# Kernel tuning notes

Hardware: AMD Instinct MI355X
Metric: run time of the kernel (lower is better)

The kernel has to match this reference:

```python
import jax, jax.numpy as jnp
import numpy as np

LEAKY_ALPHA = 0.2  # LeakyReLU negative slope from init arg `alpha`


def setup_inputs() -> dict:
    key = jax.random.key(0)
    k1, k2, k3, k4 = jax.random.split(key, 4)
    B, N, Fin, Fout = 8, 2048, 256, 256
    h = jax.random.normal(k1, (B, N, Fin), dtype=jnp.float32)
    adj = jax.random.randint(k2, (N, N), 0, 2, dtype=jnp.int32)
    W = jax.random.normal(k3, (Fin, Fout), dtype=jnp.float32) * (1.414 * (6.0 / (Fin + Fout)) ** 0.5)
    a = jax.random.normal(k4, (2 * Fout, 1), dtype=jnp.float32) * (1.414 * (6.0 / (2 * Fout + 1)) ** 0.5)
    return {"h": h, "adj": adj, "W": W, "a": a}


def reference(h, adj, W, a):
    # h: (B, N, Fin), adj: (N, N) int {0,1}, W: (Fin, Fout), a: (2*Fout, 1)
    Fout = W.shape[1]
    Wh = jnp.einsum('bnf,fo->bno', h, W)            # (B, N, Fout)
    a1 = a[:Fout, 0]                                  # attends to target node i
    a2 = a[Fout:, 0]                                  # attends to source node j
    # a^T [Wh_i || Wh_j] == (Wh_i . a1) + (Wh_j . a2); LeakyReLU applied after, as in original
    s_i = Wh @ a1                                     # (B, N)
    s_j = Wh @ a2                                     # (B, N)
    e = jax.nn.leaky_relu(s_i[:, :, None] + s_j[:, None, :], negative_slope=LEAKY_ALPHA)  # (B, N, N)
    N = Wh.shape[1]
    mask = (adj > 0) | jnp.eye(N, dtype=bool)         # adjacency + self-loops
    e = jnp.where(mask[None, :, :], e, -jnp.inf)
    attention = jax.nn.softmax(e, axis=-1)            # dropout is identity in eval
    attention = jnp.nan_to_num(attention, nan=0.0)
    h_prime = jnp.einsum('bij,bjo->bio', attention, Wh)  # (B, N, Fout)
    return jax.nn.elu(h_prime)                        # concat=True -> ELU
```

## Files before the change

kernel.cpp:

```cpp
#include <hip/hip_runtime.h>

typedef unsigned short u16;
typedef unsigned int   u32;
typedef unsigned long long u64;

typedef __bf16 bf16x8 __attribute__((ext_vector_type(8)));
typedef float  f32x4  __attribute__((ext_vector_type(4)));

#define MFMA_BF16(a,b,c) __builtin_amdgcn_mfma_f32_16x16x32_bf16((a),(b),(c),0,0,0)

__device__ __forceinline__ float bf2f(u16 u) {
    return __uint_as_float(((u32)u) << 16);
}
__device__ __forceinline__ u16 f2bf(float x) {
    u32 u = __float_as_uint(x);
    u += 0x7fffu + ((u >> 16) & 1u);
    return (u16)(u >> 16);
}
__device__ __forceinline__ float ldany(const void* p, size_t i, int f32) {
    return f32 ? ((const float*)p)[i] : bf2f(((const u16*)p)[i]);
}
__device__ __forceinline__ int detect_f32(const u32* hw) {
    u32 w = hw[threadIdx.x & 63];
    int e = (w >> 23) & 0xFF;
    u64 m = __ballot(e >= 64 && e <= 190);
    return __popcll(m) >= 32 ? 1 : 0;
}

__global__ __launch_bounds__(256) void kprep(const void* __restrict__ w, const void* __restrict__ a,
                                             const int* __restrict__ adj,
                                             u16* __restrict__ wt, float* __restrict__ wa1,
                                             float* __restrict__ wa2, u64* __restrict__ mb64,
                                             int* __restrict__ cnt, const u32* __restrict__ hw) {
    __shared__ float s1[4], s2[4];
    int bid = blockIdx.x, t = threadIdx.x;
    int wid = t >> 6, lane = t & 63;
    if (bid < 256) {
        if (bid == 0 && t < 8) cnt[t] = 0;
        int f32 = detect_f32(hw);
        int k = bid, o = t;
        float wv = ldany(w, (size_t)k * 256 + o, f32);
        wt[o * 256 + k] = f2bf(wv);
        float p1 = wv * ldany(a, o, f32);
        float p2 = wv * ldany(a, 256 + o, f32);
        for (int d = 32; d; d >>= 1) { p1 += __shfl_down(p1, d); p2 += __shfl_down(p2, d); }
        if (lane == 0) { s1[wid] = p1; s2[wid] = p2; }
        __syncthreads();
        if (o == 0) { wa1[k] = s1[0] + s1[1] + s1[2] + s1[3]; wa2[k] = s2[0] + s2[1] + s2[2] + s2[3]; }
    } else {
        int b2 = bid - 256;
        #pragma unroll
        for (int q = 0; q < 4; q++) {
            int idx = b2 * 16 + wid * 4 + q;
            int mrow = idx >> 5, c = idx & 31;
            int j = c * 64 + lane;
            bool bit = (adj[(size_t)mrow * 2048 + j] > 0) || (j == mrow);
            u64 m = __ballot(bit);
            if (lane == 0) mb64[(size_t)mrow * 32 + c] = m;
        }
    }
}

struct __align__(16) K2LDS {
    u16 At[64 * 68];
    union { u16 Bt[256 * 68]; u16 Ct[256 * 68]; };
    float wa1s[256], wa2s[256];
    float s1[64], s2[64];
};
__global__ __launch_bounds__(512) void k2(const void* __restrict__ h, const u16* __restrict__ wt,
                                          const float* __restrict__ wa1, const float* __restrict__ wa2,
                                          u16* __restrict__ whbt,
                                          float* __restrict__ sig, float* __restrict__ sjg) {
    __shared__ K2LDS L;
    int f32 = detect_f32((const u32*)h);
    int m0 = blockIdx.x * 64;
    int b  = m0 >> 11;
    int n0 = m0 & 2047;
    int t = threadIdx.x;
    int wid = t >> 6, lane = t & 63, ln = lane & 15, qd = lane >> 4;

    if (t < 256) { L.wa1s[t] = wa1[t]; L.wa2s[t] = wa2[t]; }
    if (t < 64) { L.s1[t] = 0.f; L.s2[t] = 0.f; }
    __syncthreads();

    float a1 = 0.f, a2 = 0.f;

    f32x4 acc[4][2];
    for (int mi = 0; mi < 4; mi++)
        for (int ni = 0; ni < 2; ni++)
            acc[mi][ni] = (f32x4){0.f, 0.f, 0.f, 0.f};

    for (int c = 0; c < 4; c++) {
        int k0c = c * 64;
        {
            int r = t >> 3, s = t & 7;
            float xv[8]; u16 uv[8];
            if (f32) {
                const float* src = (const float*)h + (size_t)(m0 + r) * 256 + k0c + s * 8;
                f32x4 x0 = *(const f32x4*)src;
                f32x4 x1 = *(const f32x4*)(src + 4);
                #pragma unroll
                for (int q = 0; q < 4; q++) { xv[q] = x0[q]; xv[4 + q] = x1[q]; }
                #pragma unroll
                for (int q = 0; q < 8; q++) uv[q] = f2bf(xv[q]);
            } else {
                const u16* src = (const u16*)h + (size_t)(m0 + r) * 256 + k0c + s * 8;
                *(uint4*)uv = *(const uint4*)src;
                #pragma unroll
                for (int q = 0; q < 8; q++) xv[q] = bf2f(uv[q]);
            }
            *(uint4*)&L.At[r * 68 + s * 8] = *(uint4*)uv;
            float pa = 0.f, pb = 0.f;
            #pragma unroll
            for (int q = 0; q < 8; q++) {
                pa += xv[q] * L.wa1s[k0c + s * 8 + q];
                pb += xv[q] * L.wa2s[k0c + s * 8 + q];
            }
            a1 += pa; a2 += pb;
        }
        #pragma unroll
        for (int p = 0; p < 4; p++) {
            int f = (t >> 3) + p * 64, s = t & 7;
            *(uint4*)&L.Bt[f * 68 + s * 8] =
                *(const uint4*)(wt + (size_t)f * 256 + k0c + s * 8);
        }
        __syncthreads();
        for (int ks = 0; ks < 2; ks++) {
            bf16x8 af[4], bfr[2];
            for (int mi = 0; mi < 4; mi++)
                af[mi] = *(const bf16x8*)&L.At[(mi * 16 + ln) * 68 + ks * 32 + qd * 8];
            for (int ni = 0; ni < 2; ni++)
                bfr[ni] = *(const bf16x8*)&L.Bt[(wid * 32 + ni * 16 + ln) * 68 + ks * 32 + qd * 8];
            for (int mi = 0; mi < 4; mi++)
                for (int ni = 0; ni < 2; ni++)
                    acc[mi][ni] = MFMA_BF16(af[mi], bfr[ni], acc[mi][ni]);
        }
        __syncthreads();
    }

    atomicAdd(&L.s1[t >> 3], a1);
    atomicAdd(&L.s2[t >> 3], a2);

    for (int mi = 0; mi < 4; mi++) {
        for (int ni = 0; ni < 2; ni++) {
            int f = wid * 32 + ni * 16 + ln;
            int n = mi * 16 + qd * 4;
            u16 v[4];
            for (int r = 0; r < 4; r++) v[r] = f2bf(acc[mi][ni][r]);
            *(uint2*)&L.Ct[f * 68 + n] = *(uint2*)v;
        }
    }
    __syncthreads();
    if (t < 64) { sig[m0 + t] = L.s1[t]; sjg[m0 + t] = L.s2[t]; }
    {
        int fr = t >> 1, hf = t & 1;
        size_t base = (size_t)b * 524288 + (size_t)fr * 2048 + n0;
        #pragma unroll
        for (int k = 0; k < 4; k++) {
            int s = hf * 4 + k;
            uint4 v = *(uint4*)&L.Ct[fr * 68 + s * 8];
            *(uint4*)(whbt + base + s * 8) = v;
        }
    }
}

struct __align__(16) K4LDS {
    u32   vpack[2048];
    u16   sjb[2048];
    u64   mw[64 * 33];
    float u1[64], u2[64], nsi[64], inv[64];
    float lred[1024];
    u16   Pt[2][8192];
    int   claim[2];
};
__global__ __launch_bounds__(1024, 4) void k4(const float* __restrict__ sig,
                                              const float* __restrict__ sjg,
                                              const u64* __restrict__ mb64, const u16* __restrict__ whbt,
                                              void* __restrict__ out, const void* __restrict__ hdet,
                                              int* __restrict__ cnt) {
    __shared__ K4LDS L;
    int f32 = detect_f32((const u32*)hdet);
    int t = threadIdx.x;
    if (t == 0) {
        int xcd = __builtin_amdgcn_s_getreg(63508) & 7;
        int bsel = 0, tile = 0;
        #pragma unroll
        for (int k = 0; k < 8; k++) {
            int bb = (xcd + k) & 7;
            int tt = atomicAdd(&cnt[bb], 1);
            if (tt < 32) { bsel = bb; tile = tt; break; }
        }
        L.claim[0] = bsel; L.claim[1] = tile;
    }
    __syncthreads();
    int b  = L.claim[0];
    int i0 = L.claim[1] * 64;
    int wid = t >> 6, lane = t & 63, ln = lane & 15, qd = lane >> 4;
    const u16* wb = whbt + (size_t)b * 524288 + (size_t)wid * 16 * 2048;
    float lacc = 0.f;

    bf16x8 br[2][4];
    #define LOAD_B(cc, bb) do {                                             \
        int j0_ = (cc) * 128;                                               \
        _Pragma("unroll")                                                   \
        for (int ks = 0; ks < 4; ks++)                                      \
            br[bb][ks] = *(const bf16x8*)(wb +                              \
                (size_t)ln * 2048 + j0_ + ks * 32 + qd * 8);                \
    } while (0)

    #define PGEN(cc, bb) do {                                               \
        int r_ = t & 63, o_ = t >> 6;                                       \
        int jb_ = (cc) * 128 + o_ * 8;                                      \
        uint4 pkA_ = *(const uint4*)&L.vpack[jb_];                          \
        uint4 pkB_ = *(const uint4*)&L.vpack[jb_ + 4];                      \
        uint4 sj4_ = *(const uint4*)&L.sjb[jb_];                            \
        u32 mb_ = (u32)(L.mw[r_ * 33 + 2 * (cc) + (o_ >> 3)]                \
                        >> ((o_ & 7) * 8)) & 0xffu;                         \
        float u1_ = L.u1[r_], u2_ = L.u2[r_], nsi_ = L.nsi[r_];             \
        u32 pr_[4];                                                         \
        _Pragma("unroll")                                                   \
        for (int pk = 0; pk < 4; pk++) {                                    \
            u32 vw0_ = (pk == 0) ? pkA_.x : (pk == 1) ? pkA_.z              \
                     : (pk == 2) ? pkB_.x : pkB_.z;                         \
            u32 vw1_ = (pk == 0) ? pkA_.y : (pk == 1) ? pkA_.w              \
                     : (pk == 2) ? pkB_.y : pkB_.w;                         \
            u32 sw_ = (pk == 0) ? sj4_.x : (pk == 1) ? sj4_.y               \
                     : (pk == 2) ? sj4_.z : sj4_.w;                         \
            float sj0_ = __uint_as_float(sw_ << 16);                        \
            float sj1_ = __uint_as_float(sw_ & 0xffff0000u);                \
            float p0_, p1_;                                                 \
            {                                                               \
                bool pos = sj0_ > nsi_;                                     \
                float vv = __uint_as_float(pos ? (vw0_ << 16)               \
                                               : ((vw0_ >> 16) << 16));     \
                p0_ = (pos ? u1_ : u2_) * vv;                               \
                p0_ = ((mb_ >> (2 * pk)) & 1u) ? p0_ : 0.f;                 \
            }                                                               \
            {                                                               \
                bool pos = sj1_ > nsi_;                                     \
                float vv = __uint_as_float(pos ? (vw1_ << 16)               \
                                               : ((vw1_ >> 16) << 16));     \
                p1_ = (pos ? u1_ : u2_) * vv;                               \
                p1_ = ((mb_ >> (2 * pk + 1)) & 1u) ? p1_ : 0.f;             \
            }                                                               \
            lacc += p0_ + p1_;                                              \
            pr_[pk] = __builtin_amdgcn_perm(__float_as_uint(p1_),           \
                                            __float_as_uint(p0_),           \
                                            0x07060302u);                   \
        }                                                                   \
        *(uint4*)&L.Pt[bb][t * 8] = *(uint4*)pr_;                           \
    } while (0)

    LOAD_B(0, 0);
    float sjv0 = sjg[b * 2048 + t];
    float sjv1 = sjg[b * 2048 + 1024 + t];
    {
        float mx = fmaxf(sjv0, sjv1);
        for (int d = 32; d; d >>= 1) mx = fmaxf(mx, __shfl_xor(mx, d));
        if (lane == 0) L.lred[wid] = mx;
    }
    for (int p = 0; p < 2; p++) {
        int idx = t + p * 1024;
        int r = idx >> 5, c = idx & 31;
        L.mw[r * 33 + c] = mb64[(size_t)(i0 + r) * 32 + c];
    }
    __syncthreads();
    float Mb;
    {
        float m0_ = fmaxf(fmaxf(fmaxf(L.lred[0], L.lred[1]), fmaxf(L.lred[2], L.lred[3])),
                          fmaxf(fmaxf(L.lred[4], L.lred[5]), fmaxf(L.lred[6], L.lred[7])));
        float m1_ = fmaxf(fmaxf(fmaxf(L.lred[8], L.lred[9]), fmaxf(L.lred[10], L.lred[11])),
                          fmaxf(fmaxf(L.lred[12], L.lred[13]), fmaxf(L.lred[14], L.lred[15])));
        Mb = fmaxf(m0_, m1_);
    }
    {
        float vj0 = __expf(sjv0 - Mb), v2j0 = __expf(0.2f * (sjv0 - Mb));
        L.vpack[t] = (u32)f2bf(vj0) | ((u32)f2bf(v2j0) << 16);
        L.sjb[t] = f2bf(sjv0);
        float vj1 = __expf(sjv1 - Mb), v2j1 = __expf(0.2f * (sjv1 - Mb));
        L.vpack[t + 1024] = (u32)f2bf(vj1) | ((u32)f2bf(v2j1) << 16);
        L.sjb[t + 1024] = f2bf(sjv1);
    }
    if (t < 64) {
        float siv = sig[b * 2048 + i0 + t];
        float x = siv + Mb;
        float K = fmaxf(x, 0.2f * x);
        L.u1[t] = __expf(x - K);
        L.u2[t] = __expf(0.2f * x - K);
        L.nsi[t] = -siv;
    }
    __syncthreads();
    PGEN(0, 0);

    f32x4 acc[4];
    for (int mi = 0; mi < 4; mi++)
        acc[mi] = (f32x4){0.f, 0.f, 0.f, 0.f};

    #define STEP(c, cur, nxt) do {                                          \
        __syncthreads();                                                    \
        if ((c) < 15) { LOAD_B((c) + 1, nxt); PGEN((c) + 1, nxt); }         \
        __builtin_amdgcn_s_setprio(1);                                      \
        _Pragma("unroll")                                                   \
        for (int ks = 0; ks < 4; ks++) {                                    \
            bf16x8 af[4];                                                   \
            _Pragma("unroll")                                               \
            for (int mi = 0; mi < 4; mi++)                                  \
                af[mi] = *(const bf16x8*)&L.Pt[cur][((ks * 4 + qd) * 64 +   \
                                                     mi * 16 + ln) * 8];    \
            _Pragma("unroll")                                               \
            for (int mi = 0; mi < 4; mi++)                                  \
                acc[mi] = MFMA_BF16(af[mi], br[cur][ks], acc[mi]);          \
        }                                                                   \
        __builtin_amdgcn_s_setprio(0);                                      \
    } while (0)

    for (int cc = 0; cc < 8; cc++) {
        STEP(2 * cc,     0, 1);
        STEP(2 * cc + 1, 1, 0);
    }

    __syncthreads();
    L.lred[t] = lacc;
    __syncthreads();
    if (t < 64) {
        float s = 0.f;
        #pragma unroll
        for (int q = 0; q < 16; q++) s += L.lred[q * 64 + t];
        L.inv[t] = 1.0f / s;
    }
    __syncthreads();

    {
        int fg = wid * 16 + ln;
        for (int mi = 0; mi < 4; mi++) {
            for (int reg = 0; reg < 4; reg++) {
                int rl = mi * 16 + qd * 4 + reg;
                float hp = acc[mi][reg] * L.inv[rl];
                float y = hp > 0.f ? hp : (__expf(hp) - 1.f);
                size_t idx = (size_t)(b * 2048 + i0 + rl) * 256 + fg;
                if (f32) ((float*)out)[idx] = y;
                else     ((u16*)out)[idx]   = f2bf(y);
            }
        }
    }
    #undef LOAD_B
    #undef PGEN
    #undef STEP
}

extern "C" void kernel_launch(void* const* d_in, const int* in_sizes, int n_in,
                              void* d_out, int out_size, void* d_ws, size_t ws_size,
                              hipStream_t stream) {
    const void* h   = d_in[0];
    const int*  adj = (const int*)d_in[1];
    const void* W   = d_in[2];
    const void* a   = d_in[3];

    char* ws = (char*)d_ws;
    u16*   WT    = (u16*)  (ws + 0);
    float* si    = (float*)(ws + 131072);
    float* sj    = (float*)(ws + 196608);
    u64*   mb64  = (u64*)  (ws + 557056);
    u16*   whbt  = (u16*)  (ws + 1081344);
    float* Wa1   = (float*)(ws + 9469952);
    float* Wa2   = (float*)(ws + 9470976);
    int*   cnt   = (int*)  (ws + 9472000);

    kprep<<<dim3(4352), dim3(256),  0, stream>>>(W, a, adj, WT, Wa1, Wa2, mb64, cnt, (const u32*)h);
    k2   <<<dim3(256),  dim3(512),  0, stream>>>(h, WT, Wa1, Wa2, whbt, si, sj);
    k4   <<<dim3(256),  dim3(1024), 0, stream>>>(si, sj, mb64, whbt, d_out, h, cnt);
}
```

Baseline: 132.8 us.

## Vectorize adjacency bitmask packing and split k2 loads across 1024 threads

The adjacency mask pass now loads four ints per lane with int4 loads and packs the bits with xor-shuffles instead of one-int-per-lane ballots, which halves the prep grid. k2 doubles its block to 1024 threads: the first half stages h and computes the attention projections while the second half stages W, and each wave owns one 16-column MFMA slice. The aim is more memory parallelism and less per-thread serial work in the two early kernels, at the cost of higher register pressure under the launch bound and more shuffle traffic.

New measurement: 130.7 us (median of 3 runs). No clear change (-1.6%).

```diff
diff --git a/kernel.cpp b/kernel.cpp
--- a/kernel.cpp
+++ b/kernel.cpp
@@ -48,15 +48,34 @@
         __syncthreads();
         if (o == 0) { wa1[k] = s1[0] + s1[1] + s1[2] + s1[3]; wa2[k] = s2[0] + s2[1] + s2[2] + s2[3]; }
     } else {
-        int b2 = bid - 256;
-        #pragma unroll
-        for (int q = 0; q < 4; q++) {
-            int idx = b2 * 16 + wid * 4 + q;
-            int mrow = idx >> 5, c = idx & 31;
-            int j = c * 64 + lane;
-            bool bit = (adj[(size_t)mrow * 2048 + j] > 0) || (j == mrow);
-            u64 m = __ballot(bit);
-            if (lane == 0) mb64[(size_t)mrow * 32 + c] = m;
+        int w2 = (bid - 256) * 4 + wid;
+        int4 v[2]; int rowv[2], jbv[2];
+        #pragma unroll
+        for (int s = 0; s < 2; s++) {
+            int task = w2 * 2 + s;
+            int row = task >> 3, jb = (task & 7) * 256;
+            rowv[s] = row; jbv[s] = jb;
+            v[s] = *(const int4*)(adj + (size_t)row * 2048 + jb + lane * 4);
+        }
+        #pragma unroll
+        for (int s = 0; s < 2; s++) {
+            int row = rowv[s], jb = jbv[s];
+            int j0 = jb + lane * 4;
+            u32 nib = (u32)(v[s].x > 0 || j0     == row)
+                    | ((u32)(v[s].y > 0 || j0 + 1 == row) << 1)
+                    | ((u32)(v[s].z > 0 || j0 + 2 == row) << 2)
+                    | ((u32)(v[s].w > 0 || j0 + 3 == row) << 3);
+            u32 sh = 4 * (lane & 7);
+            u32 lo = (lane & 8) ? 0u : (nib << sh);
+            u32 hi = (lane & 8) ? (nib << sh) : 0u;
+            #pragma unroll
+            for (int d = 1; d <= 8; d <<= 1) {
+                lo |= __shfl_xor(lo, d);
+                hi |= __shfl_xor(hi, d);
+            }
+            if ((lane & 15) == 0)
+                mb64[(size_t)row * 32 + (jb >> 6) + (lane >> 4)] =
+                    (u64)lo | ((u64)hi << 32);
         }
     }
 }
@@ -67,10 +86,10 @@
     float wa1s[256], wa2s[256];
     float s1[64], s2[64];
 };
-__global__ __launch_bounds__(512) void k2(const void* __restrict__ h, const u16* __restrict__ wt,
-                                          const float* __restrict__ wa1, const float* __restrict__ wa2,
-                                          u16* __restrict__ whbt,
-                                          float* __restrict__ sig, float* __restrict__ sjg) {
+__global__ __launch_bounds__(1024, 4) void k2(const void* __restrict__ h, const u16* __restrict__ wt,
+                                              const float* __restrict__ wa1, const float* __restrict__ wa2,
+                                              u16* __restrict__ whbt,
+                                              float* __restrict__ sig, float* __restrict__ sjg) {
     __shared__ K2LDS L;
     int f32 = detect_f32((const u32*)h);
     int m0 = blockIdx.x * 64;
@@ -84,15 +103,12 @@
     __syncthreads();
 
     float a1 = 0.f, a2 = 0.f;
-
-    f32x4 acc[4][2];
-    for (int mi = 0; mi < 4; mi++)
-        for (int ni = 0; ni < 2; ni++)
-            acc[mi][ni] = (f32x4){0.f, 0.f, 0.f, 0.f};
+    f32x4 acc[4];
+    for (int mi = 0; mi < 4; mi++) acc[mi] = (f32x4){0.f, 0.f, 0.f, 0.f};
 
     for (int c = 0; c < 4; c++) {
         int k0c = c * 64;
-        {
+        if (t < 512) {
             int r = t >> 3, s = t & 7;
             float xv[8]; u16 uv[8];
             if (f32) {
@@ -117,47 +133,46 @@
                 pb += xv[q] * L.wa2s[k0c + s * 8 + q];
             }
             a1 += pa; a2 += pb;
-        }
-        #pragma unroll
-        for (int p = 0; p < 4; p++) {
-            int f = (t >> 3) + p * 64, s = t & 7;
-            *(uint4*)&L.Bt[f * 68 + s * 8] =
-                *(const uint4*)(wt + (size_t)f * 256 + k0c + s * 8);
+        } else {
+            int tt = t - 512;
+            #pragma unroll
+            for (int p = 0; p < 4; p++) {
+                int f = (tt >> 3) + p * 64, s = tt & 7;
+                *(uint4*)&L.Bt[f * 68 + s * 8] =
+                    *(const uint4*)(wt + (size_t)f * 256 + k0c + s * 8);
+            }
         }
         __syncthreads();
         for (int ks = 0; ks < 2; ks++) {
-            bf16x8 af[4], bfr[2];
+            bf16x8 af[4], bfr;
             for (int mi = 0; mi < 4; mi++)
                 af[mi] = *(const bf16x8*)&L.At[(mi * 16 + ln) * 68 + ks * 32 + qd * 8];
-            for (int ni = 0; ni < 2; ni++)
-                bfr[ni] = *(const bf16x8*)&L.Bt[(wid * 32 + ni * 16 + ln) * 68 + ks * 32 + qd * 8];
+            bfr = *(const bf16x8*)&L.Bt[(wid * 16 + ln) * 68 + ks * 32 + qd * 8];
             for (int mi = 0; mi < 4; mi++)
-                for (int ni = 0; ni < 2; ni++)
-                    acc[mi][ni] = MFMA_BF16(af[mi], bfr[ni], acc[mi][ni]);
+                acc[mi] = MFMA_BF16(af[mi], bfr, acc[mi]);
         }
         __syncthreads();
     }
 
-    atomicAdd(&L.s1[t >> 3], a1);
-    atomicAdd(&L.s2[t >> 3], a2);
-
+    if (t < 512) {
+        atomicAdd(&L.s1[t >> 3], a1);
+        atomicAdd(&L.s2[t >> 3], a2);
+    }
     for (int mi = 0; mi < 4; mi++) {
-        for (int ni = 0; ni < 2; ni++) {
-            int f = wid * 32 + ni * 16 + ln;
-            int n = mi * 16 + qd * 4;
-            u16 v[4];
-            for (int r = 0; r < 4; r++) v[r] = f2bf(acc[mi][ni][r]);
-            *(uint2*)&L.Ct[f * 68 + n] = *(uint2*)v;
-        }
+        int f = wid * 16 + ln;
+        int n = mi * 16 + qd * 4;
+        u16 v[4];
+        for (int r = 0; r < 4; r++) v[r] = f2bf(acc[mi][r]);
+        *(uint2*)&L.Ct[f * 68 + n] = *(uint2*)v;
     }
     __syncthreads();
     if (t < 64) { sig[m0 + t] = L.s1[t]; sjg[m0 + t] = L.s2[t]; }
     {
-        int fr = t >> 1, hf = t & 1;
+        int fr = t >> 2, q0 = (t & 3) * 2;
         size_t base = (size_t)b * 524288 + (size_t)fr * 2048 + n0;
         #pragma unroll
-        for (int k = 0; k < 4; k++) {
-            int s = hf * 4 + k;
+        for (int k = 0; k < 2; k++) {
+            int s = q0 + k;
             uint4 v = *(uint4*)&L.Ct[fr * 68 + s * 8];
             *(uint4*)(whbt + base + s * 8) = v;
         }
@@ -366,7 +381,7 @@
     float* Wa2   = (float*)(ws + 9470976);
     int*   cnt   = (int*)  (ws + 9472000);
 
-    kprep<<<dim3(4352), dim3(256),  0, stream>>>(W, a, adj, WT, Wa1, Wa2, mb64, cnt, (const u32*)h);
-    k2   <<<dim3(256),  dim3(512),  0, stream>>>(h, WT, Wa1, Wa2, whbt, si, sj);
+    kprep<<<dim3(2304), dim3(256),  0, stream>>>(W, a, adj, WT, Wa1, Wa2, mb64, cnt, (const u32*)h);
+    k2   <<<dim3(256),  dim3(1024), 0, stream>>>(h, WT, Wa1, Wa2, whbt, si, sj);
     k4   <<<dim3(256),  dim3(1024), 0, stream>>>(si, sj, mb64, whbt, d_out, h, cnt);
 }
```
